# Performance work log

Hardware: AMD Instinct MI355X
Metric: run time of the kernel (lower is better)

Reference implementation:

```python
import jax, jax.numpy as jnp
import numpy as np

N_GROUPS = 8
TOPK = 8
ROUTE_SCALE = 2.5


def _gate(x, weight, bias):
    # scores: [N, E] via router linear, sigmoid score_func
    scores = jax.nn.sigmoid(x @ weight.T + bias)
    original_scores = scores
    n = x.shape[0]
    g = scores.reshape(n, N_GROUPS, -1)              # [N, G, E/G]
    # bias is not None -> group score = sum of top-2 expert scores per group
    top2, _ = jax.lax.top_k(g, 2)                    # [N, G, 2]
    group_scores = top2.sum(axis=-1)                 # [N, G]
    topk_groups = TOPK // N_GROUPS                   # = 1
    _, gidx = jax.lax.top_k(group_scores, topk_groups)   # [N, topk_groups]
    keep = jnp.zeros((n, N_GROUPS), dtype=bool).at[
        jnp.arange(n)[:, None], gidx].set(True)      # selected groups
    masked = jnp.where(keep[:, :, None], g, -jnp.inf).reshape(n, -1)  # [N, E]
    _, idx = jax.lax.top_k(masked, TOPK)             # [N, TOPK]
    w = jnp.take_along_axis(original_scores, idx, axis=1)
    w = w / w.sum(axis=-1, keepdims=True)            # sigmoid -> renormalize
    w = (w * ROUTE_SCALE).astype(x.dtype)
    return w, idx


def setup_inputs() -> dict:
    key = jax.random.key(0)
    kx, kw, kb = jax.random.split(key, 3)
    x = jax.random.normal(kx, (8192, 7168), dtype=jnp.float32)
    weight = jax.random.normal(kw, (256, 7168), dtype=jnp.float32) * 0.02
    bias = jax.random.normal(kb, (256,), dtype=jnp.float32) * 0.02
    return {"x": x, "weight": weight, "bias": bias}


def reference(x, weight, bias):
    return _gate(x, weight, bias)
```

## Files before the change

### kernel.cpp

```cpp
#include <hip/hip_runtime.h>
#include <math.h>

#define M 8192
#define N 256
#define K 7168
#define N_GROUPS 8
#define TOPK 8
#define ROUTE_SCALE 2.5f

#define BM 64
#define BN 128
#define BK 64

typedef _Float16 half8 __attribute__((ext_vector_type(8)));
typedef _Float16 half4 __attribute__((ext_vector_type(4)));
typedef float f32x4 __attribute__((ext_vector_type(4)));

__device__ __forceinline__ void gload_lds16(const void* g, void* l) {
    __builtin_amdgcn_global_load_lds(
        (const __attribute__((address_space(1))) unsigned int*)g,
        (__attribute__((address_space(3))) unsigned int*)l,
        16, 0, 0);
}

__global__ __launch_bounds__(256) void zero_p(float4* __restrict__ P) {
    P[blockIdx.x * 256 + threadIdx.x] = float4{0.f, 0.f, 0.f, 0.f};
}

__global__ __launch_bounds__(256) void convert_w(
        const float* __restrict__ W, _Float16* __restrict__ Wh,
        _Float16* __restrict__ Wl) {
    const int idx = blockIdx.x * 256 + threadIdx.x;
    const float4 w = ((const float4*)W)[idx];
    const float e[4] = {w.x, w.y, w.z, w.w};
    half4 h, l;
#pragma unroll
    for (int j = 0; j < 4; ++j) {
        const _Float16 hv = (_Float16)e[j];
        h[j] = hv;
        l[j] = (_Float16)(e[j] - (float)hv);
    }
    ((half4*)Wh)[idx] = h;
    ((half4*)Wl)[idx] = l;
}

__global__ __launch_bounds__(256, 3) void gemm_split(
        const float* __restrict__ X,
        const _Float16* __restrict__ Wh,
        const _Float16* __restrict__ Wl,
        float* __restrict__ P) {
    __shared__ _Float16 Ah[BM][BK], Al[BM][BK];
    __shared__ _Float16 Bh[BN][BK], Bl[BN][BK];

    const int tid = threadIdx.x;
    const int bid = blockIdx.x;
    const int x3 = bid & 7;
    const int nb = (bid >> 3) & 1;
    const int r = bid >> 4;
    const int ks = r % 3;
    const int mb = ((r / 3) << 3) | x3;
    const int m0 = mb * BM, n0 = nb * BN;
    const int kstart = (ks == 0) ? 0 : (ks == 1 ? 38 : 75);
    const int nsteps = (ks == 0) ? 38 : 37;

    const int lane = tid & 63, wave = tid >> 6;
    const int wr = wave >> 1, wc = wave & 1;
    const int lrow = lane & 15, lkq = lane >> 4;

    const int blr = lane >> 3;
    const int bcsw = (lane & 7) ^ blr;

    const int ar = tid >> 2;
    const int ac0 = (tid & 3) << 1;

    f32x4 acc[2][4];
#pragma unroll
    for (int i = 0; i < 2; ++i)
#pragma unroll
        for (int j = 0; j < 4; ++j) acc[i][j] = (f32x4){0.f, 0.f, 0.f, 0.f};

    const float* Abase = X + (size_t)(m0 + ar) * K + ac0 * 8;
    const _Float16* Whb = Wh + bcsw * 8;
    const _Float16* Wlb = Wl + bcsw * 8;

    for (int t = 0; t < nsteps; ++t) {
        const int k0 = (kstart + t) * BK;
        __syncthreads();
#pragma unroll
        for (int i = 0; i < 4; ++i) {
            const int r8 = wave * 4 + i;
            const int lr = r8 * 8 + blr;
            const size_t go = (size_t)(n0 + lr) * K + k0;
            gload_lds16(Whb + go, &Bh[r8 * 8][0]);
            gload_lds16(Wlb + go, &Bl[r8 * 8][0]);
        }
        const float* ga = Abase + k0;
        float4 f[4];
#pragma unroll
        for (int i = 0; i < 4; ++i) f[i] = ((const float4*)ga)[i];
#pragma unroll
        for (int c = 0; c < 2; ++c) {
            const float e[8] = {f[c*2].x, f[c*2].y, f[c*2].z, f[c*2].w,
                                f[c*2+1].x, f[c*2+1].y, f[c*2+1].z, f[c*2+1].w};
            half8 h, l;
#pragma unroll
            for (int j = 0; j < 8; ++j) {
                const _Float16 hv = (_Float16)e[j];
                h[j] = hv;
                l[j] = (_Float16)(e[j] - (float)hv);
            }
            const int p = (ac0 + c) ^ (ar & 7);
            *(half8*)&Ah[ar][p * 8] = h;
            *(half8*)&Al[ar][p * 8] = l;
        }
        __syncthreads();

#pragma unroll
        for (int s = 0; s < 2; ++s) {
            const int pc8 = ((s * 4 + lkq) ^ (lrow & 7)) * 8;
            const half8 ah0 = *(const half8*)&Ah[wr*32 + lrow][pc8];
            const half8 ah1 = *(const half8*)&Ah[wr*32 + 16 + lrow][pc8];
            const half8 al0 = *(const half8*)&Al[wr*32 + lrow][pc8];
            const half8 al1 = *(const half8*)&Al[wr*32 + 16 + lrow][pc8];
#pragma unroll
            for (int j = 0; j < 4; ++j) {
                const int br = wc*64 + j*16 + lrow;
                const half8 bh = *(const half8*)&Bh[br][pc8];
                const half8 bl = *(const half8*)&Bl[br][pc8];
                acc[0][j] = __builtin_amdgcn_mfma_f32_16x16x32_f16(ah0, bh, acc[0][j], 0, 0, 0);
                acc[1][j] = __builtin_amdgcn_mfma_f32_16x16x32_f16(ah1, bh, acc[1][j], 0, 0, 0);
                acc[0][j] = __builtin_amdgcn_mfma_f32_16x16x32_f16(ah0, bl, acc[0][j], 0, 0, 0);
                acc[1][j] = __builtin_amdgcn_mfma_f32_16x16x32_f16(ah1, bl, acc[1][j], 0, 0, 0);
                acc[0][j] = __builtin_amdgcn_mfma_f32_16x16x32_f16(al0, bh, acc[0][j], 0, 0, 0);
                acc[1][j] = __builtin_amdgcn_mfma_f32_16x16x32_f16(al1, bh, acc[1][j], 0, 0, 0);
            }
        }
    }

#pragma unroll
    for (int i = 0; i < 2; ++i) {
        const int row = m0 + wr * 32 + i * 16 + lkq * 4;
#pragma unroll
        for (int j = 0; j < 4; ++j) {
            const int col = n0 + wc * 64 + j * 16 + lrow;
#pragma unroll
            for (int rr = 0; rr < 4; ++rr)
                atomicAdd(&P[(size_t)(row + rr) * N + col], acc[i][j][rr]);
        }
    }
}

__global__ __launch_bounds__(256) void gate_topk(
        const float* __restrict__ P, const float* __restrict__ bias,
        float* __restrict__ out_w, float* __restrict__ out_i) {
    const int row = blockIdx.x * 4 + (threadIdx.x >> 6);
    const int lane = threadIdx.x & 63;

    const float4 a4 = *reinterpret_cast<const float4*>(P + (size_t)row * N + lane * 4);
    const float4 bb = *reinterpret_cast<const float4*>(bias + lane * 4);
    float v[4] = {1.f / (1.f + expf(-(a4.x + bb.x))),
                  1.f / (1.f + expf(-(a4.y + bb.y))),
                  1.f / (1.f + expf(-(a4.z + bb.z))),
                  1.f / (1.f + expf(-(a4.w + bb.w)))};

    float t1 = v[0], t2 = -1.f;
#pragma unroll
    for (int j = 1; j < 4; ++j) {
        if (v[j] > t1) { t2 = t1; t1 = v[j]; }
        else if (v[j] > t2) { t2 = v[j]; }
    }
#pragma unroll
    for (int m = 1; m <= 4; m <<= 1) {
        const float o1 = __shfl_xor(t1, m, 64);
        const float o2 = __shfl_xor(t2, m, 64);
        const float n1 = fmaxf(t1, o1);
        const float n2 = fmaxf(fminf(t1, o1), fmaxf(t2, o2));
        t1 = n1; t2 = n2;
    }
    float gs = t1 + t2;
    int gid = lane >> 3;
#pragma unroll
    for (int m = 8; m <= 32; m <<= 1) {
        const float og = __shfl_xor(gs, m, 64);
        const int oi = __shfl_xor(gid, m, 64);
        if (og > gs || (og == gs && oi < gid)) { gs = og; gid = oi; }
    }

    const bool inG = ((lane >> 3) == gid);
    if (!inG) { v[0] = v[1] = v[2] = v[3] = -1.f; }

    float wv[8];
    int wi[8];
#pragma unroll
    for (int r = 0; r < 8; ++r) {
        float bv = v[0]; int bj = 0;
#pragma unroll
        for (int j = 1; j < 4; ++j)
            if (v[j] > bv) { bv = v[j]; bj = j; }
        int be = lane * 4 + bj;
#pragma unroll
        for (int m = 1; m <= 32; m <<= 1) {
            const float ov = __shfl_xor(bv, m, 64);
            const int oe = __shfl_xor(be, m, 64);
            if (ov > bv || (ov == bv && oe < be)) { bv = ov; be = oe; }
        }
        wv[r] = bv; wi[r] = be;
        if ((be >> 2) == lane) v[be & 3] = -1.f;
    }

    float sum = 0.f;
#pragma unroll
    for (int r = 0; r < 8; ++r) sum += wv[r];

    if (lane == 0) {
#pragma unroll
        for (int r = 0; r < 8; ++r) {
            out_w[(size_t)row * TOPK + r] = wv[r] / sum * ROUTE_SCALE;
            out_i[(size_t)row * TOPK + r] = (float)wi[r];
        }
    }
}

extern "C" void kernel_launch(void* const* d_in, const int* in_sizes, int n_in,
                              void* d_out, int out_size, void* d_ws, size_t ws_size,
                              hipStream_t stream) {
    const float* x = (const float*)d_in[0];
    const float* w = (const float*)d_in[1];
    const float* b = (const float*)d_in[2];

    char* ws = (char*)d_ws;
    _Float16* Wh = (_Float16*)ws;
    _Float16* Wl = (_Float16*)(ws + 3670016);
    float* P = (float*)(ws + 7340032);

    float* out_w = (float*)d_out;
    float* out_i = out_w + (size_t)M * TOPK;

    zero_p<<<(M * N / 4) / 256, 256, 0, stream>>>((float4*)P);
    convert_w<<<(N * K / 4) / 256, 256, 0, stream>>>(w, Wh, Wl);
    gemm_split<<<768, 256, 0, stream>>>(x, Wh, Wl, P);
    gate_topk<<<M / 4, 256, 0, stream>>>(P, b, out_w, out_i);
}
```

Measured before the change: 402.0 us.

## Enlarge GEMM M-tile to 128, split K four ways, prefetch X tile into registers

The M tile grows from 64 to 128 rows, so each wave computes a 4x4 grid of MFMA tiles and reuses each B fragment across more rows. K is now split four ways with 28 steps each instead of three uneven splits, and the launch drops to 512 blocks with an occupancy hint of 2. The next step's fp32 X tile is loaded into registers during the current step's MFMA work, hiding global load latency. The cost is much higher register pressure and fewer resident blocks, plus more atomic partial sums per output element.

```diff
diff --git a/kernel.cpp b/kernel.cpp
--- a/kernel.cpp
+++ b/kernel.cpp
@@ -8,9 +8,11 @@
 #define TOPK 8
 #define ROUTE_SCALE 2.5f
 
-#define BM 64
+#define BM 128
 #define BN 128
 #define BK 64
+#define KSPLIT 4
+#define NSTEPS 28
 
 typedef _Float16 half8 __attribute__((ext_vector_type(8)));
 typedef _Float16 half4 __attribute__((ext_vector_type(4)));
@@ -44,24 +46,22 @@
     ((half4*)Wl)[idx] = l;
 }
 
-__global__ __launch_bounds__(256, 3) void gemm_split(
+__global__ __launch_bounds__(256, 2) void gemm_split(
         const float* __restrict__ X,
         const _Float16* __restrict__ Wh,
         const _Float16* __restrict__ Wl,
         float* __restrict__ P) {
-    __shared__ _Float16 Ah[BM][BK], Al[BM][BK];
-    __shared__ _Float16 Bh[BN][BK], Bl[BN][BK];
+    __shared__ __align__(16) _Float16 Ah[BM][BK], Al[BM][BK];
+    __shared__ __align__(16) _Float16 Bh[BN][BK], Bl[BN][BK];
 
     const int tid = threadIdx.x;
     const int bid = blockIdx.x;
     const int x3 = bid & 7;
-    const int nb = (bid >> 3) & 1;
-    const int r = bid >> 4;
-    const int ks = r % 3;
-    const int mb = ((r / 3) << 3) | x3;
+    const int rest = bid >> 3;
+    const int nb = rest & 1;
+    const int ks = (rest >> 1) & 3;
+    const int mb = ((rest >> 3) << 3) | x3;
     const int m0 = mb * BM, n0 = nb * BN;
-    const int kstart = (ks == 0) ? 0 : (ks == 1 ? 38 : 75);
-    const int nsteps = (ks == 0) ? 38 : 37;
 
     const int lane = tid & 63, wave = tid >> 6;
     const int wr = wave >> 1, wc = wave & 1;
@@ -70,21 +70,25 @@
     const int blr = lane >> 3;
     const int bcsw = (lane & 7) ^ blr;
 
-    const int ar = tid >> 2;
-    const int ac0 = (tid & 3) << 1;
-
-    f32x4 acc[2][4];
-#pragma unroll
-    for (int i = 0; i < 2; ++i)
+    const int ar = tid >> 1;
+    const int ahalf = tid & 1;
+
+    f32x4 acc[4][4];
+#pragma unroll
+    for (int i = 0; i < 4; ++i)
 #pragma unroll
         for (int j = 0; j < 4; ++j) acc[i][j] = (f32x4){0.f, 0.f, 0.f, 0.f};
 
-    const float* Abase = X + (size_t)(m0 + ar) * K + ac0 * 8;
+    const float* Abase = X + (size_t)(m0 + ar) * K + ahalf * 32 + ks * (NSTEPS * BK);
     const _Float16* Whb = Wh + bcsw * 8;
     const _Float16* Wlb = Wl + bcsw * 8;
 
-    for (int t = 0; t < nsteps; ++t) {
-        const int k0 = (kstart + t) * BK;
+    float4 f[8];
+#pragma unroll
+    for (int i = 0; i < 8; ++i) f[i] = ((const float4*)Abase)[i];
+
+    for (int t = 0; t < NSTEPS; ++t) {
+        const int k0 = (ks * NSTEPS + t) * BK;
         __syncthreads();
 #pragma unroll
         for (int i = 0; i < 4; ++i) {
@@ -94,12 +98,8 @@
             gload_lds16(Whb + go, &Bh[r8 * 8][0]);
             gload_lds16(Wlb + go, &Bl[r8 * 8][0]);
         }
-        const float* ga = Abase + k0;
-        float4 f[4];
-#pragma unroll
-        for (int i = 0; i < 4; ++i) f[i] = ((const float4*)ga)[i];
-#pragma unroll
-        for (int c = 0; c < 2; ++c) {
+#pragma unroll
+        for (int c = 0; c < 4; ++c) {
             const float e[8] = {f[c*2].x, f[c*2].y, f[c*2].z, f[c*2].w,
                                 f[c*2+1].x, f[c*2+1].y, f[c*2+1].z, f[c*2+1].w};
             half8 h, l;
@@ -109,43 +109,53 @@
                 h[j] = hv;
                 l[j] = (_Float16)(e[j] - (float)hv);
             }
-            const int p = (ac0 + c) ^ (ar & 7);
+            const int p = (ahalf * 4 + c) ^ (ar & 7);
             *(half8*)&Ah[ar][p * 8] = h;
             *(half8*)&Al[ar][p * 8] = l;
         }
         __syncthreads();
 
+        if (t + 1 < NSTEPS) {
+            const float* ga = Abase + (t + 1) * BK;
+#pragma unroll
+            for (int i = 0; i < 8; ++i) f[i] = ((const float4*)ga)[i];
+        }
+
 #pragma unroll
         for (int s = 0; s < 2; ++s) {
-            const int pc8 = ((s * 4 + lkq) ^ (lrow & 7)) * 8;
-            const half8 ah0 = *(const half8*)&Ah[wr*32 + lrow][pc8];
-            const half8 ah1 = *(const half8*)&Ah[wr*32 + 16 + lrow][pc8];
-            const half8 al0 = *(const half8*)&Al[wr*32 + lrow][pc8];
-            const half8 al1 = *(const half8*)&Al[wr*32 + 16 + lrow][pc8];
-#pragma unroll
-            for (int j = 0; j < 4; ++j) {
-                const int br = wc*64 + j*16 + lrow;
-                const half8 bh = *(const half8*)&Bh[br][pc8];
-                const half8 bl = *(const half8*)&Bl[br][pc8];
-                acc[0][j] = __builtin_amdgcn_mfma_f32_16x16x32_f16(ah0, bh, acc[0][j], 0, 0, 0);
-                acc[1][j] = __builtin_amdgcn_mfma_f32_16x16x32_f16(ah1, bh, acc[1][j], 0, 0, 0);
-                acc[0][j] = __builtin_amdgcn_mfma_f32_16x16x32_f16(ah0, bl, acc[0][j], 0, 0, 0);
-                acc[1][j] = __builtin_amdgcn_mfma_f32_16x16x32_f16(ah1, bl, acc[1][j], 0, 0, 0);
-                acc[0][j] = __builtin_amdgcn_mfma_f32_16x16x32_f16(al0, bh, acc[0][j], 0, 0, 0);
-                acc[1][j] = __builtin_amdgcn_mfma_f32_16x16x32_f16(al1, bh, acc[1][j], 0, 0, 0);
+            half8 ah[4], al[4];
+#pragma unroll
+            for (int mi = 0; mi < 4; ++mi) {
+                const int arow = wr * 64 + mi * 16 + lrow;
+                const int pc8 = ((s * 4 + lkq) ^ (arow & 7)) * 8;
+                ah[mi] = *(const half8*)&Ah[arow][pc8];
+                al[mi] = *(const half8*)&Al[arow][pc8];
             }
-        }
-    }
-
-#pragma unroll
-    for (int i = 0; i < 2; ++i) {
-        const int row = m0 + wr * 32 + i * 16 + lkq * 4;
-#pragma unroll
-        for (int j = 0; j < 4; ++j) {
-            const int col = n0 + wc * 64 + j * 16 + lrow;
+#pragma unroll
+            for (int nj = 0; nj < 4; ++nj) {
+                const int brow = wc * 64 + nj * 16 + lrow;
+                const int pc8 = ((s * 4 + lkq) ^ (brow & 7)) * 8;
+                const half8 bh = *(const half8*)&Bh[brow][pc8];
+                const half8 bl = *(const half8*)&Bl[brow][pc8];
+#pragma unroll
+                for (int mi = 0; mi < 4; ++mi) {
+                    acc[mi][nj] = __builtin_amdgcn_mfma_f32_16x16x32_f16(ah[mi], bh, acc[mi][nj], 0, 0, 0);
+                    acc[mi][nj] = __builtin_amdgcn_mfma_f32_16x16x32_f16(ah[mi], bl, acc[mi][nj], 0, 0, 0);
+                    acc[mi][nj] = __builtin_amdgcn_mfma_f32_16x16x32_f16(al[mi], bh, acc[mi][nj], 0, 0, 0);
+                }
+            }
+        }
+    }
+
+#pragma unroll
+    for (int mi = 0; mi < 4; ++mi) {
+        const int row = m0 + wr * 64 + mi * 16 + lkq * 4;
+#pragma unroll
+        for (int nj = 0; nj < 4; ++nj) {
+            const int col = n0 + wc * 64 + nj * 16 + lrow;
 #pragma unroll
             for (int rr = 0; rr < 4; ++rr)
-                atomicAdd(&P[(size_t)(row + rr) * N + col], acc[i][j][rr]);
+                atomicAdd(&P[(size_t)(row + rr) * N + col], acc[mi][nj][rr]);
         }
     }
 }
@@ -238,6 +248,6 @@
 
     zero_p<<<(M * N / 4) / 256, 256, 0, stream>>>((float4*)P);
     convert_w<<<(N * K / 4) / 256, 256, 0, stream>>>(w, Wh, Wl);
-    gemm_split<<<768, 256, 0, stream>>>(x, Wh, Wl, P);
+    gemm_split<<<512, 256, 0, stream>>>(x, Wh, Wl, P);
     gate_topk<<<M / 4, 256, 0, stream>>>(P, b, out_w, out_i);
 }
```

New measurement: 407.1 us. Within noise of the previous version (+1.3%).
